# Optimization experiments

Hardware: AMD Instinct MI355X
Metric: run time of the kernel (lower is better)

Reference implementation:

```python
import jax, jax.numpy as jnp
import numpy as np

# Grid / model dims
B, H, W = 1, 90, 180
P = H * W                 # 16200 spatial points
MODEL_DIM = 130
L = MODEL_DIM - 2         # learnable_dim = 128
NH, HD = 8, 16            # n_heads, head_dim
S = 16                    # shared_hidden (DISCO out_channels)
K = 25                    # number of DISCO basis functions (piecewise-linear 5x5)
NNB = 25                  # neighbors per output point (theta_cutoff stencil)
MH = 32                   # head MLP hidden
FH = 256                  # FFN hidden


def setup_inputs() -> dict:
    key = jax.random.key(0)
    ks = jax.random.split(key, 12)
    x = jax.random.normal(ks[0], (B, H, W, MODEL_DIM), dtype=jnp.float32)
    # sparse DISCO structure: neighbor indices + precomputed (quadrature-weighted) basis values
    nbr_idx = jax.random.randint(ks[1], (P, NNB), 0, P, dtype=jnp.int32)
    basis_vals = jax.random.normal(ks[2], (K, P, NNB), dtype=jnp.float32) * 0.1
    # learnable DISCO kernel weights (out_channels=S, in_channels=1, K basis coeffs) + bias
    disco_w = jax.random.normal(ks[3], (S, K), dtype=jnp.float32) / np.sqrt(K).astype(np.float32)
    disco_b = jax.random.normal(ks[4], (S,), dtype=jnp.float32) * 0.01
    # per-head MLP params: S -> MH -> 1, one set per head
    head_w1 = jax.random.normal(ks[5], (NH, S, MH), dtype=jnp.float32) / np.sqrt(S).astype(np.float32)
    head_b1 = jnp.zeros((NH, MH), dtype=jnp.float32)
    head_w2 = jax.random.normal(ks[6], (NH, MH, 1), dtype=jnp.float32) / np.sqrt(MH).astype(np.float32)
    head_b2 = jnp.zeros((NH, 1), dtype=jnp.float32)
    # FFN: model_dim -> FH -> L, with the sin/cos input columns zeroed (as in __init__)
    ffn_w1 = jax.random.normal(ks[7], (MODEL_DIM, FH), dtype=jnp.float32) / np.sqrt(MODEL_DIM).astype(np.float32)
    ffn_w1 = ffn_w1.at[-2:, :].set(0.0)
    ffn_b1 = jnp.zeros((FH,), dtype=jnp.float32)
    ffn_w2 = jax.random.normal(ks[8], (FH, L), dtype=jnp.float32) / np.sqrt(FH).astype(np.float32)
    ffn_b2 = jnp.zeros((L,), dtype=jnp.float32)
    return dict(x=x, nbr_idx=nbr_idx, basis_vals=basis_vals, disco_w=disco_w, disco_b=disco_b,
                head_w1=head_w1, head_b1=head_b1, head_w2=head_w2, head_b2=head_b2,
                ffn_w1=ffn_w1, ffn_b1=ffn_b1, ffn_w2=ffn_w2, ffn_b2=ffn_b2)


def reference(x, nbr_idx, basis_vals, disco_w, disco_b,
              head_w1, head_b1, head_w2, head_b2,
              ffn_w1, ffn_b1, ffn_w2, ffn_b2):
    gelu = lambda t: jax.nn.gelu(t, approximate=False)  # torch nn.GELU default is exact
    x_learn = x[..., :L]          # (B,H,W,L)
    sin_cos = x[..., L:]          # (B,H,W,2)
    x_res = x_learn

    # ---- DISCO spherical conv, depthwise over B*L channels (in_channels=1) ----
    xf = jnp.transpose(x_learn, (0, 3, 1, 2)).reshape(B * L, P)      # (N, P)
    gathered = xf[:, nbr_idx]                                        # (N, P, NNB) irregular gather
    z = jnp.einsum('kpn,cpn->ckp', basis_vals, gathered)             # (N, K, P) basis projections
    y = jnp.einsum('sk,ckp->csp', disco_w, z) + disco_b[None, :, None]  # (N, S, P)
    disco_out = y.reshape(B, L, S, H, W).transpose(0, 3, 4, 1, 2)    # (B,H,W,L,S)

    # ---- per-head MLP, vectorized over heads ----
    hfeat = disco_out.reshape(B, H, W, NH, HD, S)                    # (B,H,W,NH,HD,S)
    h1 = gelu(jnp.einsum('bxyhds,hsm->bxyhdm', hfeat, head_w1) + head_b1[:, None, :])
    hout = jnp.einsum('bxyhdm,hmo->bxyhdo', h1, head_w2) + head_b2[:, None, :]  # o=1
    x_mix = hout.reshape(B, H, W, L)                                 # heads concatenated in order
    x_mix = x_mix + x_res                                            # residual

    # ---- FFN channel mixing on [x_mix, sin_cos] ----
    x_full = jnp.concatenate([x_mix, sin_cos], axis=-1)              # (B,H,W,MODEL_DIM)
    hf = gelu(jnp.einsum('bxyd,df->bxyf', x_full, ffn_w1) + ffn_b1)
    x_ffn = jnp.einsum('bxyf,fl->bxyl', hf, ffn_w2) + ffn_b2
    x_out = x_ffn + x_mix
    return jnp.concatenate([x_out, sin_cos], axis=-1)                # (B,H,W,MODEL_DIM)
```

## Files before the change

### kernel.cpp

```cpp
#include <hip/hip_runtime.h>
#include <hip/hip_bf16.h>

#define P_TOT 16200
#define MODEL_DIMC 130
#define L_DIM 128
#define NHH 8
#define S_DIM 16
#define K_DIM 25
#define NNBC 25
#define MH_DIM 32
#define FH_DIM 256

__device__ __forceinline__ float gelu_f(float x) {
    float z = fabsf(x) * 0.70710678118654752440f;
    float t = __builtin_amdgcn_rcpf(fmaf(0.3275911f, z, 1.0f));
    float poly = t * fmaf(t, fmaf(t, fmaf(t, fmaf(t, 1.061405429f, -1.453152027f),
                                          1.421413741f), -0.284496736f), 0.254829592f);
    float e = __expf(-z * z);
    float erfp = fmaf(-poly, e, 1.0f);
    float erfv = copysignf(erfp, x);
    return 0.5f * x * (1.0f + erfv);
}

__global__ __launch_bounds__(256) void k0_transpose_w1(const float* __restrict__ hw1,
                                                       float* __restrict__ w1t) {
    int i = blockIdx.x * 256 + threadIdx.x;
    if (i < NHH * S_DIM * MH_DIM) {
        int h = i >> 9, s = (i >> 5) & 15, m = i & 31;
        w1t[h * 512 + m * 16 + s] = hw1[i];
    }
}

__global__ __launch_bounds__(256) void k1_bw(const float* __restrict__ basis,
                                             const float* __restrict__ disco_w,
                                             float* __restrict__ bw) {
    __shared__ float w[S_DIM * K_DIM];
    int tid = threadIdx.x;
    for (int i = tid; i < S_DIM * K_DIM; i += 256) w[i] = disco_w[i];
    __syncthreads();
    int i = blockIdx.x * 256 + tid;
    if (i >= P_TOT * NNBC) return;
    float bv[K_DIM];
#pragma unroll
    for (int k = 0; k < K_DIM; k++) bv[k] = basis[k * (P_TOT * NNBC) + i];
    float acc[S_DIM];
#pragma unroll
    for (int s = 0; s < S_DIM; s++) {
        float a = 0.f;
#pragma unroll
        for (int k = 0; k < K_DIM; k++) a = fmaf(w[s * K_DIM + k], bv[k], a);
        acc[s] = a;
    }
    float4* outp = (float4*)(bw + (size_t)i * S_DIM);
#pragma unroll
    for (int q = 0; q < 4; q++) {
        float4 v; v.x = acc[q*4+0]; v.y = acc[q*4+1]; v.z = acc[q*4+2]; v.w = acc[q*4+3];
        outp[q] = v;
    }
}

#define YSTR 2056
__global__ __launch_bounds__(256, 2) void k2_disco_head(
        const float* __restrict__ x, const int* __restrict__ nbr,
        const float* __restrict__ bw, const float* __restrict__ w1t,
        const float* __restrict__ head_b1, const float* __restrict__ head_w2,
        const float* __restrict__ head_b2, const float* __restrict__ disco_b,
        float* __restrict__ xmix) {
    __shared__ float ylds[4 * YSTR];

    int tid  = threadIdx.x;
    int lane = tid & 63;
    int wv   = __builtin_amdgcn_readfirstlane(tid >> 6);
    int p0   = blockIdx.x * 4;
    int p    = p0 + wv;

    const float* bwp = bw + (size_t)p * (NNBC * S_DIM);
    const int*   nbp = nbr + p * NNBC;

    int un[NNBC];
#pragma unroll
    for (int j = 0; j < NNBC; j++) un[j] = nbp[j];

    float y0[16], y1[16];
#pragma unroll
    for (int s = 0; s < 16; s++) { float db = disco_b[s]; y0[s] = db; y1[s] = db; }

    const float* xb0 = x + lane;
    const float* xb1 = x + 64 + lane;

#pragma unroll 1
    for (int nb = 0; nb < 24; nb += 2) {
        int u0 = un[nb], u1 = un[nb + 1];
        float g00 = xb0[(size_t)u0 * MODEL_DIMC];
        float g01 = xb1[(size_t)u0 * MODEL_DIMC];
        float g10 = xb0[(size_t)u1 * MODEL_DIMC];
        float g11 = xb1[(size_t)u1 * MODEL_DIMC];
#pragma unroll
        for (int s = 0; s < 16; s++) {
            float w0 = bwp[nb * 16 + s];
            float w1_ = bwp[nb * 16 + 16 + s];
            y0[s] = fmaf(g00, w0, y0[s]);
            y1[s] = fmaf(g01, w0, y1[s]);
            y0[s] = fmaf(g10, w1_, y0[s]);
            y1[s] = fmaf(g11, w1_, y1[s]);
        }
    }
    {
        int u = un[24];
        float g0 = xb0[(size_t)u * MODEL_DIMC];
        float g1 = xb1[(size_t)u * MODEL_DIMC];
#pragma unroll
        for (int s = 0; s < 16; s++) {
            float wv_ = bwp[24 * 16 + s];
            y0[s] = fmaf(g0, wv_, y0[s]);
            y1[s] = fmaf(g1, wv_, y1[s]);
        }
    }

#pragma unroll
    for (int s = 0; s < 16; s++) {
        ylds[wv * YSTR + s * 128 + lane]      = y0[s];
        ylds[wv * YSTR + s * 128 + 64 + lane] = y1[s];
    }
    __syncthreads();

    int ptl = lane >> 4;
    int d   = lane & 15;
#pragma unroll
    for (int t = 0; t < 2; t++) {
        int hh = __builtin_amdgcn_readfirstlane(wv + 4 * t);
        float yv[16];
#pragma unroll
        for (int s = 0; s < 16; s++)
            yv[s] = ylds[ptl * YSTR + s * 128 + hh * 16 + d];
        const float* wrow = w1t + hh * (MH_DIM * S_DIM);
        const float* b1r  = head_b1 + hh * MH_DIM;
        const float* w2r  = head_w2 + hh * MH_DIM;
        float acc = head_b2[hh];
#pragma unroll 2
        for (int m = 0; m < MH_DIM; m++) {
            float a = b1r[m];
#pragma unroll
            for (int s = 0; s < 16; s++)
                a = fmaf(yv[s], wrow[m * 16 + s], a);
            a = gelu_f(a);
            acc = fmaf(a, w2r[m], acc);
        }
        int pp = p0 + ptl;
        int c  = hh * 16 + d;
        xmix[pp * L_DIM + c] = acc + x[(size_t)pp * MODEL_DIMC + c];
    }
}

__global__ __launch_bounds__(256, 2) void k3a_ffn1(
        const float* __restrict__ xmix, const float* __restrict__ w1,
        const float* __restrict__ b1, float* __restrict__ hf) {
    __shared__ __align__(16) float xm[16 * 132];
    int tid = threadIdx.x;
    int p0 = blockIdx.x * 16;
    int valid = min(16, P_TOT - p0);
    {
        const float4* src = (const float4*)(xmix + (size_t)p0 * L_DIM);
        for (int j = tid; j < valid * 32; j += 256) {
            float4 v = src[j];
            int pt = j >> 5, q = j & 31;
            *(float4*)&xm[pt * 132 + q * 4] = v;
        }
    }
    __syncthreads();

    int fid = tid & 63, pid = tid >> 6;
    int f0 = fid * 4;
    float4 bb = *(const float4*)&b1[f0];
    float acc[4][4];
#pragma unroll
    for (int i = 0; i < 4; i++) {
        acc[i][0] = bb.x; acc[i][1] = bb.y; acc[i][2] = bb.z; acc[i][3] = bb.w;
    }
#pragma unroll 2
    for (int k0 = 0; k0 < 128; k0 += 4) {
        float4 w4[4];
#pragma unroll
        for (int j = 0; j < 4; j++)
            w4[j] = *(const float4*)&w1[(k0 + j) * FH_DIM + f0];
#pragma unroll
        for (int i = 0; i < 4; i++) {
            float4 xv = *(const float4*)&xm[(pid * 4 + i) * 132 + k0];
            acc[i][0] = fmaf(xv.x, w4[0].x, acc[i][0]);
            acc[i][1] = fmaf(xv.x, w4[0].y, acc[i][1]);
            acc[i][2] = fmaf(xv.x, w4[0].z, acc[i][2]);
            acc[i][3] = fmaf(xv.x, w4[0].w, acc[i][3]);
            acc[i][0] = fmaf(xv.y, w4[1].x, acc[i][0]);
            acc[i][1] = fmaf(xv.y, w4[1].y, acc[i][1]);
            acc[i][2] = fmaf(xv.y, w4[1].z, acc[i][2]);
            acc[i][3] = fmaf(xv.y, w4[1].w, acc[i][3]);
            acc[i][0] = fmaf(xv.z, w4[2].x, acc[i][0]);
            acc[i][1] = fmaf(xv.z, w4[2].y, acc[i][1]);
            acc[i][2] = fmaf(xv.z, w4[2].z, acc[i][2]);
            acc[i][3] = fmaf(xv.z, w4[2].w, acc[i][3]);
            acc[i][0] = fmaf(xv.w, w4[3].x, acc[i][0]);
            acc[i][1] = fmaf(xv.w, w4[3].y, acc[i][1]);
            acc[i][2] = fmaf(xv.w, w4[3].z, acc[i][2]);
            acc[i][3] = fmaf(xv.w, w4[3].w, acc[i][3]);
        }
    }
#pragma unroll
    for (int i = 0; i < 4; i++) {
        int pl = pid * 4 + i;
        if (pl < valid) {
            float4 v;
            v.x = gelu_f(acc[i][0]);
            v.y = gelu_f(acc[i][1]);
            v.z = gelu_f(acc[i][2]);
            v.w = gelu_f(acc[i][3]);
            *(float4*)&hf[(size_t)(p0 + pl) * FH_DIM + f0] = v;
        }
    }
}

__global__ __launch_bounds__(256, 2) void k3b_ffn2(
        const float* __restrict__ x, const float* __restrict__ xmix,
        const float* __restrict__ hf, const float* __restrict__ w2,
        const float* __restrict__ b2, float* __restrict__ out) {
    __shared__ __align__(16) float hfl[16 * 264];
    int tid = threadIdx.x;
    int p0 = blockIdx.x * 16;
    int valid = min(16, P_TOT - p0);
    {
        const float4* src = (const float4*)(hf + (size_t)p0 * FH_DIM);
        for (int j = tid; j < valid * 64; j += 256) {
            float4 v = src[j];
            int pt = j >> 6, q = j & 63;
            *(float4*)&hfl[pt * 264 + q * 4] = v;
        }
    }
    __syncthreads();

    int lid = tid & 31, pid = tid >> 5;
    int l0 = lid * 4;
    float4 bb = *(const float4*)&b2[l0];
    float acc[2][4];
#pragma unroll
    for (int i = 0; i < 2; i++) {
        acc[i][0] = bb.x; acc[i][1] = bb.y; acc[i][2] = bb.z; acc[i][3] = bb.w;
    }
#pragma unroll 2
    for (int f0 = 0; f0 < FH_DIM; f0 += 4) {
        float4 w4[4];
#pragma unroll
        for (int j = 0; j < 4; j++)
            w4[j] = *(const float4*)&w2[(f0 + j) * L_DIM + l0];
#pragma unroll
        for (int i = 0; i < 2; i++) {
            float4 hv = *(const float4*)&hfl[(pid * 2 + i) * 264 + f0];
            acc[i][0] = fmaf(hv.x, w4[0].x, acc[i][0]);
            acc[i][1] = fmaf(hv.x, w4[0].y, acc[i][1]);
            acc[i][2] = fmaf(hv.x, w4[0].z, acc[i][2]);
            acc[i][3] = fmaf(hv.x, w4[0].w, acc[i][3]);
            acc[i][0] = fmaf(hv.y, w4[1].x, acc[i][0]);
            acc[i][1] = fmaf(hv.y, w4[1].y, acc[i][1]);
            acc[i][2] = fmaf(hv.y, w4[1].z, acc[i][2]);
            acc[i][3] = fmaf(hv.y, w4[1].w, acc[i][3]);
            acc[i][0] = fmaf(hv.z, w4[2].x, acc[i][0]);
            acc[i][1] = fmaf(hv.z, w4[2].y, acc[i][1]);
            acc[i][2] = fmaf(hv.z, w4[2].z, acc[i][2]);
            acc[i][3] = fmaf(hv.z, w4[2].w, acc[i][3]);
            acc[i][0] = fmaf(hv.w, w4[3].x, acc[i][0]);
            acc[i][1] = fmaf(hv.w, w4[3].y, acc[i][1]);
            acc[i][2] = fmaf(hv.w, w4[3].z, acc[i][2]);
            acc[i][3] = fmaf(hv.w, w4[3].w, acc[i][3]);
        }
    }
#pragma unroll
    for (int i = 0; i < 2; i++) {
        int pl = pid * 2 + i;
        if (pl < valid) {
            int pp = p0 + pl;
            float4 xm4 = *(const float4*)&xmix[(size_t)pp * L_DIM + l0];
            float2 o01, o23;
            o01.x = acc[i][0] + xm4.x;
            o01.y = acc[i][1] + xm4.y;
            o23.x = acc[i][2] + xm4.z;
            o23.y = acc[i][3] + xm4.w;
            *(float2*)&out[(size_t)pp * MODEL_DIMC + l0]     = o01;
            *(float2*)&out[(size_t)pp * MODEL_DIMC + l0 + 2] = o23;
        }
    }
    if (tid < 32) {
        int pt = tid >> 1, wch = tid & 1;
        if (pt < valid) {
            int pp = p0 + pt;
            out[(size_t)pp * MODEL_DIMC + 128 + wch] = x[(size_t)pp * MODEL_DIMC + 128 + wch];
        }
    }
}

extern "C" void kernel_launch(void* const* d_in, const int* in_sizes, int n_in,
                              void* d_out, int out_size, void* d_ws, size_t ws_size,
                              hipStream_t stream) {
    const float* x        = (const float*)d_in[0];
    const int*   nbr      = (const int*)  d_in[1];
    const float* basis    = (const float*)d_in[2];
    const float* disco_w  = (const float*)d_in[3];
    const float* disco_b  = (const float*)d_in[4];
    const float* head_w1  = (const float*)d_in[5];
    const float* head_b1  = (const float*)d_in[6];
    const float* head_w2  = (const float*)d_in[7];
    const float* head_b2  = (const float*)d_in[8];
    const float* ffn_w1   = (const float*)d_in[9];
    const float* ffn_b1   = (const float*)d_in[10];
    const float* ffn_w2   = (const float*)d_in[11];
    const float* ffn_b2   = (const float*)d_in[12];
    float* out = (float*)d_out;

    float* bw   = (float*)d_ws;
    float* xmix = bw + (size_t)P_TOT * NNBC * S_DIM;
    float* w1t  = xmix + (size_t)P_TOT * L_DIM;
    float* hf   = bw;

    hipLaunchKernelGGL(k0_transpose_w1, dim3(16), dim3(256), 0, stream, head_w1, w1t);
    hipLaunchKernelGGL(k1_bw, dim3((P_TOT * NNBC + 255) / 256), dim3(256), 0, stream,
                       basis, disco_w, bw);
    hipLaunchKernelGGL(k2_disco_head, dim3(P_TOT / 4), dim3(256), 0, stream,
                       x, nbr, bw, w1t, head_b1, head_w2, head_b2, disco_b, xmix);
    hipLaunchKernelGGL(k3a_ffn1, dim3((P_TOT + 15) / 16), dim3(256), 0, stream,
                       xmix, ffn_w1, ffn_b1, hf);
    hipLaunchKernelGGL(k3b_ffn2, dim3((P_TOT + 15) / 16), dim3(256), 0, stream,
                       x, xmix, hf, ffn_w2, ffn_b2, out);
}
```

Before: 272.8 us.

## Fuse FFN kernels, merge transpose into bw kernel, retune disco-head occupancy

Merges the w1 transpose into the basis-weight kernel as extra blocks, removing one launch. Fuses the two FFN kernels so the hidden activations stay in shared memory instead of round-tripping through global memory, and reuses the staged xmix for the residual. Raises the disco-head kernel's occupancy target, drops the neighbor index register array, rotates LDS columns to avoid bank conflicts, and splits the head MLP dot product into two accumulator chains. The higher occupancy target may force register spills.

```diff
diff --git a/kernel.cpp b/kernel.cpp
--- a/kernel.cpp
+++ b/kernel.cpp
@@ -22,23 +22,26 @@
     return 0.5f * x * (1.0f + erfv);
 }
 
-__global__ __launch_bounds__(256) void k0_transpose_w1(const float* __restrict__ hw1,
-                                                       float* __restrict__ w1t) {
-    int i = blockIdx.x * 256 + threadIdx.x;
-    if (i < NHH * S_DIM * MH_DIM) {
-        int h = i >> 9, s = (i >> 5) & 15, m = i & 31;
-        w1t[h * 512 + m * 16 + s] = hw1[i];
-    }
-}
-
-__global__ __launch_bounds__(256) void k1_bw(const float* __restrict__ basis,
-                                             const float* __restrict__ disco_w,
-                                             float* __restrict__ bw) {
+#define NB1 1583
+__global__ __launch_bounds__(256) void k1_bw_t(const float* __restrict__ basis,
+                                               const float* __restrict__ disco_w,
+                                               const float* __restrict__ hw1,
+                                               float* __restrict__ bw,
+                                               float* __restrict__ w1t) {
+    int bid = blockIdx.x;
+    int tid = threadIdx.x;
+    if (bid >= NB1) {
+        int i = (bid - NB1) * 256 + tid;
+        if (i < NHH * S_DIM * MH_DIM) {
+            int h = i >> 9, s = (i >> 5) & 15, m = i & 31;
+            w1t[h * 512 + m * 16 + s] = hw1[i];
+        }
+        return;
+    }
     __shared__ float w[S_DIM * K_DIM];
-    int tid = threadIdx.x;
     for (int i = tid; i < S_DIM * K_DIM; i += 256) w[i] = disco_w[i];
     __syncthreads();
-    int i = blockIdx.x * 256 + tid;
+    int i = bid * 256 + tid;
     if (i >= P_TOT * NNBC) return;
     float bv[K_DIM];
 #pragma unroll
@@ -59,14 +62,13 @@
     }
 }
 
-#define YSTR 2056
-__global__ __launch_bounds__(256, 2) void k2_disco_head(
+__global__ __launch_bounds__(256, 5) void k2_disco_head(
         const float* __restrict__ x, const int* __restrict__ nbr,
         const float* __restrict__ bw, const float* __restrict__ w1t,
         const float* __restrict__ head_b1, const float* __restrict__ head_w2,
         const float* __restrict__ head_b2, const float* __restrict__ disco_b,
         float* __restrict__ xmix) {
-    __shared__ float ylds[4 * YSTR];
+    __shared__ float ylds[4 * 2048];
 
     int tid  = threadIdx.x;
     int lane = tid & 63;
@@ -77,10 +79,6 @@
     const float* bwp = bw + (size_t)p * (NNBC * S_DIM);
     const int*   nbp = nbr + p * NNBC;
 
-    int un[NNBC];
-#pragma unroll
-    for (int j = 0; j < NNBC; j++) un[j] = nbp[j];
-
     float y0[16], y1[16];
 #pragma unroll
     for (int s = 0; s < 16; s++) { float db = disco_b[s]; y0[s] = db; y1[s] = db; }
@@ -90,14 +88,14 @@
 
 #pragma unroll 1
     for (int nb = 0; nb < 24; nb += 2) {
-        int u0 = un[nb], u1 = un[nb + 1];
+        int u0 = nbp[nb], u1 = nbp[nb + 1];
         float g00 = xb0[(size_t)u0 * MODEL_DIMC];
         float g01 = xb1[(size_t)u0 * MODEL_DIMC];
         float g10 = xb0[(size_t)u1 * MODEL_DIMC];
         float g11 = xb1[(size_t)u1 * MODEL_DIMC];
 #pragma unroll
         for (int s = 0; s < 16; s++) {
-            float w0 = bwp[nb * 16 + s];
+            float w0  = bwp[nb * 16 + s];
             float w1_ = bwp[nb * 16 + 16 + s];
             y0[s] = fmaf(g00, w0, y0[s]);
             y1[s] = fmaf(g01, w0, y1[s]);
@@ -106,7 +104,7 @@
         }
     }
     {
-        int u = un[24];
+        int u = nbp[24];
         float g0 = xb0[(size_t)u * MODEL_DIMC];
         float g1 = xb1[(size_t)u * MODEL_DIMC];
 #pragma unroll
@@ -117,45 +115,63 @@
         }
     }
 
+    int cr0 = (lane + 8 * wv) & 127;
+    int cr1 = (cr0 + 64) & 127;
 #pragma unroll
     for (int s = 0; s < 16; s++) {
-        ylds[wv * YSTR + s * 128 + lane]      = y0[s];
-        ylds[wv * YSTR + s * 128 + 64 + lane] = y1[s];
+        ylds[wv * 2048 + s * 128 + cr0] = y0[s];
+        ylds[wv * 2048 + s * 128 + cr1] = y1[s];
     }
     __syncthreads();
 
     int ptl = lane >> 4;
     int d   = lane & 15;
+    int ybase = ptl * 2048;
+    int rot   = 8 * ptl;
 #pragma unroll
     for (int t = 0; t < 2; t++) {
         int hh = __builtin_amdgcn_readfirstlane(wv + 4 * t);
+        int cc  = hh * 16 + d;
+        int col = (cc + rot) & 127;
         float yv[16];
 #pragma unroll
         for (int s = 0; s < 16; s++)
-            yv[s] = ylds[ptl * YSTR + s * 128 + hh * 16 + d];
+            yv[s] = ylds[ybase + s * 128 + col];
         const float* wrow = w1t + hh * (MH_DIM * S_DIM);
         const float* b1r  = head_b1 + hh * MH_DIM;
         const float* w2r  = head_w2 + hh * MH_DIM;
         float acc = head_b2[hh];
-#pragma unroll 2
-        for (int m = 0; m < MH_DIM; m++) {
-            float a = b1r[m];
-#pragma unroll
-            for (int s = 0; s < 16; s++)
-                a = fmaf(yv[s], wrow[m * 16 + s], a);
-            a = gelu_f(a);
-            acc = fmaf(a, w2r[m], acc);
+#pragma unroll 1
+        for (int m = 0; m < MH_DIM; m += 2) {
+            const float* wm0 = wrow + m * 16;
+            const float* wm1 = wrow + m * 16 + 16;
+            float a0 = b1r[m], a1 = b1r[m + 1];
+            float a0b = 0.f, a1b = 0.f;
+#pragma unroll
+            for (int s = 0; s < 8; s++) {
+                a0  = fmaf(yv[s],     wm0[s],     a0);
+                a0b = fmaf(yv[s + 8], wm0[s + 8], a0b);
+                a1  = fmaf(yv[s],     wm1[s],     a1);
+                a1b = fmaf(yv[s + 8], wm1[s + 8], a1b);
+            }
+            a0 += a0b; a1 += a1b;
+            a0 = gelu_f(a0);
+            a1 = gelu_f(a1);
+            acc = fmaf(a0, w2r[m],     acc);
+            acc = fmaf(a1, w2r[m + 1], acc);
         }
         int pp = p0 + ptl;
-        int c  = hh * 16 + d;
-        xmix[pp * L_DIM + c] = acc + x[(size_t)pp * MODEL_DIMC + c];
-    }
-}
-
-__global__ __launch_bounds__(256, 2) void k3a_ffn1(
-        const float* __restrict__ xmix, const float* __restrict__ w1,
-        const float* __restrict__ b1, float* __restrict__ hf) {
+        xmix[pp * L_DIM + cc] = acc + x[(size_t)pp * MODEL_DIMC + cc];
+    }
+}
+
+__global__ __launch_bounds__(256) void k3_ffn(
+        const float* __restrict__ x, const float* __restrict__ xmix,
+        const float* __restrict__ w1, const float* __restrict__ b1,
+        const float* __restrict__ w2, const float* __restrict__ b2,
+        float* __restrict__ out) {
     __shared__ __align__(16) float xm[16 * 132];
+    __shared__ __align__(16) float hfl[16 * 260];
     int tid = threadIdx.x;
     int p0 = blockIdx.x * 16;
     int valid = min(16, P_TOT - p0);
@@ -169,128 +185,112 @@
     }
     __syncthreads();
 
-    int fid = tid & 63, pid = tid >> 6;
-    int f0 = fid * 4;
-    float4 bb = *(const float4*)&b1[f0];
-    float acc[4][4];
-#pragma unroll
-    for (int i = 0; i < 4; i++) {
-        acc[i][0] = bb.x; acc[i][1] = bb.y; acc[i][2] = bb.z; acc[i][3] = bb.w;
-    }
+    {
+        int fid = tid & 63, wid = tid >> 6;
+        int f0 = fid * 4;
+        float4 bb = *(const float4*)&b1[f0];
+        float acc[4][4];
+#pragma unroll
+        for (int i = 0; i < 4; i++) {
+            acc[i][0] = bb.x; acc[i][1] = bb.y; acc[i][2] = bb.z; acc[i][3] = bb.w;
+        }
 #pragma unroll 2
-    for (int k0 = 0; k0 < 128; k0 += 4) {
-        float4 w4[4];
-#pragma unroll
-        for (int j = 0; j < 4; j++)
-            w4[j] = *(const float4*)&w1[(k0 + j) * FH_DIM + f0];
+        for (int k0 = 0; k0 < 128; k0 += 4) {
+            float4 w4[4];
+#pragma unroll
+            for (int j = 0; j < 4; j++)
+                w4[j] = *(const float4*)&w1[(k0 + j) * FH_DIM + f0];
+#pragma unroll
+            for (int i = 0; i < 4; i++) {
+                float4 xv = *(const float4*)&xm[(wid * 4 + i) * 132 + k0];
+                acc[i][0] = fmaf(xv.x, w4[0].x, acc[i][0]);
+                acc[i][1] = fmaf(xv.x, w4[0].y, acc[i][1]);
+                acc[i][2] = fmaf(xv.x, w4[0].z, acc[i][2]);
+                acc[i][3] = fmaf(xv.x, w4[0].w, acc[i][3]);
+                acc[i][0] = fmaf(xv.y, w4[1].x, acc[i][0]);
+                acc[i][1] = fmaf(xv.y, w4[1].y, acc[i][1]);
+                acc[i][2] = fmaf(xv.y, w4[1].z, acc[i][2]);
+                acc[i][3] = fmaf(xv.y, w4[1].w, acc[i][3]);
+                acc[i][0] = fmaf(xv.z, w4[2].x, acc[i][0]);
+                acc[i][1] = fmaf(xv.z, w4[2].y, acc[i][1]);
+                acc[i][2] = fmaf(xv.z, w4[2].z, acc[i][2]);
+                acc[i][3] = fmaf(xv.z, w4[2].w, acc[i][3]);
+                acc[i][0] = fmaf(xv.w, w4[3].x, acc[i][0]);
+                acc[i][1] = fmaf(xv.w, w4[3].y, acc[i][1]);
+                acc[i][2] = fmaf(xv.w, w4[3].z, acc[i][2]);
+                acc[i][3] = fmaf(xv.w, w4[3].w, acc[i][3]);
+            }
+        }
 #pragma unroll
         for (int i = 0; i < 4; i++) {
-            float4 xv = *(const float4*)&xm[(pid * 4 + i) * 132 + k0];
-            acc[i][0] = fmaf(xv.x, w4[0].x, acc[i][0]);
-            acc[i][1] = fmaf(xv.x, w4[0].y, acc[i][1]);
-            acc[i][2] = fmaf(xv.x, w4[0].z, acc[i][2]);
-            acc[i][3] = fmaf(xv.x, w4[0].w, acc[i][3]);
-            acc[i][0] = fmaf(xv.y, w4[1].x, acc[i][0]);
-            acc[i][1] = fmaf(xv.y, w4[1].y, acc[i][1]);
-            acc[i][2] = fmaf(xv.y, w4[1].z, acc[i][2]);
-            acc[i][3] = fmaf(xv.y, w4[1].w, acc[i][3]);
-            acc[i][0] = fmaf(xv.z, w4[2].x, acc[i][0]);
-            acc[i][1] = fmaf(xv.z, w4[2].y, acc[i][1]);
-            acc[i][2] = fmaf(xv.z, w4[2].z, acc[i][2]);
-            acc[i][3] = fmaf(xv.z, w4[2].w, acc[i][3]);
-            acc[i][0] = fmaf(xv.w, w4[3].x, acc[i][0]);
-            acc[i][1] = fmaf(xv.w, w4[3].y, acc[i][1]);
-            acc[i][2] = fmaf(xv.w, w4[3].z, acc[i][2]);
-            acc[i][3] = fmaf(xv.w, w4[3].w, acc[i][3]);
-        }
-    }
-#pragma unroll
-    for (int i = 0; i < 4; i++) {
-        int pl = pid * 4 + i;
-        if (pl < valid) {
+            int pt = wid * 4 + i;
             float4 v;
             v.x = gelu_f(acc[i][0]);
             v.y = gelu_f(acc[i][1]);
             v.z = gelu_f(acc[i][2]);
             v.w = gelu_f(acc[i][3]);
-            *(float4*)&hf[(size_t)(p0 + pl) * FH_DIM + f0] = v;
-        }
-    }
-}
-
-__global__ __launch_bounds__(256, 2) void k3b_ffn2(
-        const float* __restrict__ x, const float* __restrict__ xmix,
-        const float* __restrict__ hf, const float* __restrict__ w2,
-        const float* __restrict__ b2, float* __restrict__ out) {
-    __shared__ __align__(16) float hfl[16 * 264];
-    int tid = threadIdx.x;
-    int p0 = blockIdx.x * 16;
-    int valid = min(16, P_TOT - p0);
+            *(float4*)&hfl[pt * 260 + f0] = v;
+        }
+    }
+    __syncthreads();
+
     {
-        const float4* src = (const float4*)(hf + (size_t)p0 * FH_DIM);
-        for (int j = tid; j < valid * 64; j += 256) {
-            float4 v = src[j];
-            int pt = j >> 6, q = j & 63;
-            *(float4*)&hfl[pt * 264 + q * 4] = v;
-        }
-    }
-    __syncthreads();
-
-    int lid = tid & 31, pid = tid >> 5;
-    int l0 = lid * 4;
-    float4 bb = *(const float4*)&b2[l0];
-    float acc[2][4];
-#pragma unroll
-    for (int i = 0; i < 2; i++) {
-        acc[i][0] = bb.x; acc[i][1] = bb.y; acc[i][2] = bb.z; acc[i][3] = bb.w;
-    }
+        int lid = tid & 31, pgb = tid >> 5;
+        int l0 = lid * 4;
+        float4 bb = *(const float4*)&b2[l0];
+        float acc[2][4];
+#pragma unroll
+        for (int i = 0; i < 2; i++) {
+            acc[i][0] = bb.x; acc[i][1] = bb.y; acc[i][2] = bb.z; acc[i][3] = bb.w;
+        }
 #pragma unroll 2
-    for (int f0 = 0; f0 < FH_DIM; f0 += 4) {
-        float4 w4[4];
-#pragma unroll
-        for (int j = 0; j < 4; j++)
-            w4[j] = *(const float4*)&w2[(f0 + j) * L_DIM + l0];
+        for (int f0 = 0; f0 < FH_DIM; f0 += 4) {
+            float4 w4[4];
+#pragma unroll
+            for (int j = 0; j < 4; j++)
+                w4[j] = *(const float4*)&w2[(f0 + j) * L_DIM + l0];
+#pragma unroll
+            for (int i = 0; i < 2; i++) {
+                float4 hv = *(const float4*)&hfl[(pgb * 2 + i) * 260 + f0];
+                acc[i][0] = fmaf(hv.x, w4[0].x, acc[i][0]);
+                acc[i][1] = fmaf(hv.x, w4[0].y, acc[i][1]);
+                acc[i][2] = fmaf(hv.x, w4[0].z, acc[i][2]);
+                acc[i][3] = fmaf(hv.x, w4[0].w, acc[i][3]);
+                acc[i][0] = fmaf(hv.y, w4[1].x, acc[i][0]);
+                acc[i][1] = fmaf(hv.y, w4[1].y, acc[i][1]);
+                acc[i][2] = fmaf(hv.y, w4[1].z, acc[i][2]);
+                acc[i][3] = fmaf(hv.y, w4[1].w, acc[i][3]);
+                acc[i][0] = fmaf(hv.z, w4[2].x, acc[i][0]);
+                acc[i][1] = fmaf(hv.z, w4[2].y, acc[i][1]);
+                acc[i][2] = fmaf(hv.z, w4[2].z, acc[i][2]);
+                acc[i][3] = fmaf(hv.z, w4[2].w, acc[i][3]);
+                acc[i][0] = fmaf(hv.w, w4[3].x, acc[i][0]);
+                acc[i][1] = fmaf(hv.w, w4[3].y, acc[i][1]);
+                acc[i][2] = fmaf(hv.w, w4[3].z, acc[i][2]);
+                acc[i][3] = fmaf(hv.w, w4[3].w, acc[i][3]);
+            }
+        }
 #pragma unroll
         for (int i = 0; i < 2; i++) {
-            float4 hv = *(const float4*)&hfl[(pid * 2 + i) * 264 + f0];
-            acc[i][0] = fmaf(hv.x, w4[0].x, acc[i][0]);
-            acc[i][1] = fmaf(hv.x, w4[0].y, acc[i][1]);
-            acc[i][2] = fmaf(hv.x, w4[0].z, acc[i][2]);
-            acc[i][3] = fmaf(hv.x, w4[0].w, acc[i][3]);
-            acc[i][0] = fmaf(hv.y, w4[1].x, acc[i][0]);
-            acc[i][1] = fmaf(hv.y, w4[1].y, acc[i][1]);
-            acc[i][2] = fmaf(hv.y, w4[1].z, acc[i][2]);
-            acc[i][3] = fmaf(hv.y, w4[1].w, acc[i][3]);
-            acc[i][0] = fmaf(hv.z, w4[2].x, acc[i][0]);
-            acc[i][1] = fmaf(hv.z, w4[2].y, acc[i][1]);
-            acc[i][2] = fmaf(hv.z, w4[2].z, acc[i][2]);
-            acc[i][3] = fmaf(hv.z, w4[2].w, acc[i][3]);
-            acc[i][0] = fmaf(hv.w, w4[3].x, acc[i][0]);
-            acc[i][1] = fmaf(hv.w, w4[3].y, acc[i][1]);
-            acc[i][2] = fmaf(hv.w, w4[3].z, acc[i][2]);
-            acc[i][3] = fmaf(hv.w, w4[3].w, acc[i][3]);
-        }
-    }
-#pragma unroll
-    for (int i = 0; i < 2; i++) {
-        int pl = pid * 2 + i;
-        if (pl < valid) {
-            int pp = p0 + pl;
-            float4 xm4 = *(const float4*)&xmix[(size_t)pp * L_DIM + l0];
-            float2 o01, o23;
-            o01.x = acc[i][0] + xm4.x;
-            o01.y = acc[i][1] + xm4.y;
-            o23.x = acc[i][2] + xm4.z;
-            o23.y = acc[i][3] + xm4.w;
-            *(float2*)&out[(size_t)pp * MODEL_DIMC + l0]     = o01;
-            *(float2*)&out[(size_t)pp * MODEL_DIMC + l0 + 2] = o23;
-        }
-    }
-    if (tid < 32) {
-        int pt = tid >> 1, wch = tid & 1;
-        if (pt < valid) {
-            int pp = p0 + pt;
-            out[(size_t)pp * MODEL_DIMC + 128 + wch] = x[(size_t)pp * MODEL_DIMC + 128 + wch];
+            int pl = pgb * 2 + i;
+            if (pl < valid) {
+                int pp = p0 + pl;
+                float4 xm4 = *(const float4*)&xm[pl * 132 + l0];
+                float2 o01, o23;
+                o01.x = acc[i][0] + xm4.x;
+                o01.y = acc[i][1] + xm4.y;
+                o23.x = acc[i][2] + xm4.z;
+                o23.y = acc[i][3] + xm4.w;
+                *(float2*)&out[(size_t)pp * MODEL_DIMC + l0]     = o01;
+                *(float2*)&out[(size_t)pp * MODEL_DIMC + l0 + 2] = o23;
+            }
+        }
+        if (tid < 32) {
+            int pt = tid >> 1, wch = tid & 1;
+            if (pt < valid) {
+                int pp = p0 + pt;
+                out[(size_t)pp * MODEL_DIMC + 128 + wch] = x[(size_t)pp * MODEL_DIMC + 128 + wch];
+            }
         }
     }
 }
@@ -316,15 +316,11 @@
     float* bw   = (float*)d_ws;
     float* xmix = bw + (size_t)P_TOT * NNBC * S_DIM;
     float* w1t  = xmix + (size_t)P_TOT * L_DIM;
-    float* hf   = bw;
-
-    hipLaunchKernelGGL(k0_transpose_w1, dim3(16), dim3(256), 0, stream, head_w1, w1t);
-    hipLaunchKernelGGL(k1_bw, dim3((P_TOT * NNBC + 255) / 256), dim3(256), 0, stream,
-                       basis, disco_w, bw);
+
+    hipLaunchKernelGGL(k1_bw_t, dim3(NB1 + 16), dim3(256), 0, stream,
+                       basis, disco_w, head_w1, bw, w1t);
     hipLaunchKernelGGL(k2_disco_head, dim3(P_TOT / 4), dim3(256), 0, stream,
                        x, nbr, bw, w1t, head_b1, head_w2, head_b2, disco_b, xmix);
-    hipLaunchKernelGGL(k3a_ffn1, dim3((P_TOT + 15) / 16), dim3(256), 0, stream,
-                       xmix, ffn_w1, ffn_b1, hf);
-    hipLaunchKernelGGL(k3b_ffn2, dim3((P_TOT + 15) / 16), dim3(256), 0, stream,
-                       x, xmix, hf, ffn_w2, ffn_b2, out);
-}
+    hipLaunchKernelGGL(k3_ffn, dim3((P_TOT + 15) / 16), dim3(256), 0, stream,
+                       x, xmix, ffn_w1, ffn_b1, ffn_w2, ffn_b2, out);
+}
```

New measurement: 269.8 us. Within noise of the previous version (-1.1%).
